# Performance work log

Hardware: AMD Instinct MI355X
Metric: run time of the kernel (lower is better)

Reference implementation:

```python
import jax, jax.numpy as jnp
import numpy as np

N, E = 50000, 800000
IN_C, HID_C, OUT_C, HEADS = 128, 32, 16, 4
NEG_SLOPE = 0.2


def gat_conv(x, src, dst, W, att_src, att_dst, bias, heads, out_ch, concat, n_nodes):
    # linear transform: [N, heads, out_ch]
    h = (x @ W).reshape(n_nodes, heads, out_ch)
    # per-node attention logits [N, heads]
    a_s = (h * att_src).sum(-1)
    a_d = (h * att_dst).sum(-1)
    # per-edge raw attention (edge j->i uses src logit of j, dst logit of i)
    alpha = jax.nn.leaky_relu(a_s[src] + a_d[dst], negative_slope=NEG_SLOPE)  # [E, heads]
    # segment softmax over destination neighborhoods
    amax = jax.ops.segment_max(alpha, dst, num_segments=n_nodes)
    ex = jnp.exp(alpha - amax[dst])
    den = jax.ops.segment_sum(ex, dst, num_segments=n_nodes)
    coef = ex / den[dst]  # [E, heads]
    # weighted scatter-add aggregation
    msg = h[src] * coef[:, :, None]  # [E, heads, out_ch]
    out = jax.ops.segment_sum(msg, dst, num_segments=n_nodes)  # [N, heads, out_ch]
    out = out.reshape(n_nodes, heads * out_ch) if concat else out.mean(axis=1)
    return out + bias


def setup_inputs() -> dict:
    key = jax.random.key(0)
    ks = jax.random.split(key, 10)
    x = jax.random.normal(ks[0], (N, IN_C), dtype=jnp.float32)
    edge_index = jax.random.randint(ks[1], (2, E), 0, N, dtype=jnp.int64)
    s1 = 1.0 / np.sqrt(IN_C)
    s2 = 1.0 / np.sqrt(HID_C * HEADS)
    W1 = jax.random.normal(ks[2], (IN_C, HEADS * HID_C), dtype=jnp.float32) * s1
    att_src1 = jax.random.normal(ks[3], (HEADS, HID_C), dtype=jnp.float32) * s1
    att_dst1 = jax.random.normal(ks[4], (HEADS, HID_C), dtype=jnp.float32) * s1
    b1 = jnp.zeros((HEADS * HID_C,), dtype=jnp.float32)
    W2 = jax.random.normal(ks[5], (HEADS * HID_C, OUT_C), dtype=jnp.float32) * s2
    att_src2 = jax.random.normal(ks[6], (1, OUT_C), dtype=jnp.float32) * s2
    att_dst2 = jax.random.normal(ks[7], (1, OUT_C), dtype=jnp.float32) * s2
    b2 = jnp.zeros((OUT_C,), dtype=jnp.float32)
    return {"x": x, "edge_index": edge_index, "W1": W1, "att_src1": att_src1,
            "att_dst1": att_dst1, "b1": b1, "W2": W2, "att_src2": att_src2,
            "att_dst2": att_dst2, "b2": b2}


def reference(x, edge_index, W1, att_src1, att_dst1, b1, W2, att_src2, att_dst2, b2):
    n = x.shape[0]
    # PyG GATConv default: add self loops
    ar = jnp.arange(n, dtype=edge_index.dtype)
    src = jnp.concatenate([edge_index[0], ar])
    dst = jnp.concatenate([edge_index[1], ar])
    h = gat_conv(x, src, dst, W1, att_src1, att_dst1, b1, HEADS, HID_C, True, n)
    h = jax.nn.elu(h)
    out = gat_conv(h, src, dst, W2, att_src2, att_dst2, b2, 1, OUT_C, False, n)
    return out
```

## Files before the change

### kernel.cpp

```cpp
#include <hip/hip_runtime.h>

typedef __attribute__((ext_vector_type(8))) short short8;
typedef __attribute__((ext_vector_type(4))) float f32x4;
typedef __attribute__((ext_vector_type(2))) float f32x2;

__device__ __forceinline__ float lrelu02(float a) { return a > 0.0f ? a : 0.2f * a; }

__device__ __forceinline__ unsigned bf16rne(float f) {
    unsigned u = __float_as_uint(f);
    return (u + 0x7fffu + ((u >> 16) & 1u)) >> 16;
}

__global__ __launch_bounds__(256) void k_rank(
    const int* __restrict__ ei, int* __restrict__ deg, int* __restrict__ rank,
    int E, int N)
{
    int tid = blockIdx.x * blockDim.x + threadIdx.x;
    int nthr = gridDim.x * blockDim.x;
    int E4 = E & ~3;
    for (int b = tid * 4; b < E4; b += nthr * 4) {
        int4 d = *(const int4*)(ei + E + b);
        int4 r;
        r.x = atomicAdd(&deg[d.x], 1);
        r.y = atomicAdd(&deg[d.y], 1);
        r.z = atomicAdd(&deg[d.z], 1);
        r.w = atomicAdd(&deg[d.w], 1);
        *(int4*)(rank + b) = r;
    }
    for (int e = E4 + tid; e < E; e += nthr)
        rank[e] = atomicAdd(&deg[ei[E + e]], 1);
    for (int i = tid; i < N; i += nthr)
        rank[E + i] = atomicAdd(&deg[i], 1);
}

__global__ __launch_bounds__(256) void k_gemm1(
    const float* __restrict__ x, const float* __restrict__ W,
    const float* __restrict__ attS, const float* __restrict__ attD,
    unsigned short* __restrict__ h1, float* __restrict__ as1, float* __restrict__ ad1,
    int4* __restrict__ degz, int n4, int N)
{
    __shared__ unsigned short Wt[128 * 128];
    __shared__ unsigned short xs[64 * 128];

    const int t = threadIdx.x;
    const int lane = t & 63;
    const int wv = t >> 6;
    const int ln = lane & 15;
    const int lg = lane >> 4;
    const int r0 = blockIdx.x * 64;

    for (int i = blockIdx.x * 256 + t; i < n4; i += gridDim.x * 256)
        degz[i] = make_int4(0, 0, 0, 0);

    #pragma unroll
    for (int i = 0; i < 16; ++i) {
        int flat = i * 256 + t;
        int n = flat & 127;
        int k0 = (flat >> 7) * 4;
        float v0 = W[(size_t)(k0 + 0) * 128 + n];
        float v1 = W[(size_t)(k0 + 1) * 128 + n];
        float v2 = W[(size_t)(k0 + 2) * 128 + n];
        float v3 = W[(size_t)(k0 + 3) * 128 + n];
        uint2 pk;
        pk.x = bf16rne(v0) | (bf16rne(v1) << 16);
        pk.y = bf16rne(v2) | (bf16rne(v3) << 16);
        int byteo = n * 256 + ((k0 * 2) ^ ((n & 7) << 4));
        *(uint2*)((char*)Wt + byteo) = pk;
    }
    {
        int mbase = t >> 5, k0 = (t & 31) * 4;
        #pragma unroll
        for (int it = 0; it < 8; ++it) {
            int m = mbase + it * 8;
            int rr = r0 + m;
            float4 v = make_float4(0.f, 0.f, 0.f, 0.f);
            if (rr < N) v = *(const float4*)&x[(size_t)rr * 128 + k0];
            unsigned lo = bf16rne(v.x) | (bf16rne(v.y) << 16);
            unsigned hi = bf16rne(v.z) | (bf16rne(v.w) << 16);
            int byteo = m * 256 + ((k0 * 2) ^ ((m & 7) << 4));
            *(uint2*)((char*)xs + byteo) = make_uint2(lo, hi);
        }
    }
    __syncthreads();

    f32x4 acc[8];
    #pragma unroll
    for (int i = 0; i < 8; ++i) acc[i] = (f32x4)(0.f);

    #pragma unroll
    for (int kk = 0; kk < 4; ++kk) {
        int kb = (kk * 32 + lg * 8) * 2;
        int am = wv * 16 + ln;
        short8 a = *(const short8*)((char*)xs + am * 256 + (kb ^ ((am & 7) << 4)));
        #pragma unroll
        for (int tile = 0; tile < 8; ++tile) {
            int n = tile * 16 + ln;
            short8 b = *(const short8*)((char*)Wt + n * 256 + (kb ^ ((n & 7) << 4)));
            acc[tile] = __builtin_amdgcn_mfma_f32_16x16x32_bf16(a, b, acc[tile], 0, 0, 0);
        }
    }

    float aSt[8], aDt[8];
    #pragma unroll
    for (int tile = 0; tile < 8; ++tile) {
        aSt[tile] = attS[tile * 16 + ln];
        aDt[tile] = attD[tile * 16 + ln];
    }
    #pragma unroll
    for (int r = 0; r < 4; ++r) {
        int row = r0 + wv * 16 + lg * 4 + r;
        #pragma unroll
        for (int h = 0; h < 4; ++h) {
            float s = acc[2*h][r] * aSt[2*h] + acc[2*h+1][r] * aSt[2*h+1];
            float d = acc[2*h][r] * aDt[2*h] + acc[2*h+1][r] * aDt[2*h+1];
            s += __shfl_xor(s, 1); s += __shfl_xor(s, 2); s += __shfl_xor(s, 4); s += __shfl_xor(s, 8);
            d += __shfl_xor(d, 1); d += __shfl_xor(d, 2); d += __shfl_xor(d, 4); d += __shfl_xor(d, 8);
            if (ln == h * 4 + r && row < N) {
                as1[row * 4 + h] = s;
                ad1[row * 4 + h] = d;
            }
        }
    }

    __syncthreads();
    #pragma unroll
    for (int tile = 0; tile < 8; ++tile) {
        #pragma unroll
        for (int r = 0; r < 4; ++r) {
            int m = wv * 16 + lg * 4 + r;
            int byteo = m * 256 + (((tile * 16 + ln) * 2) ^ ((m & 7) << 4));
            *(unsigned short*)((char*)xs + byteo) = (unsigned short)bf16rne(acc[tile][r]);
        }
    }
    __syncthreads();
    #pragma unroll
    for (int it = 0; it < 4; ++it) {
        int idx = t + it * 256;
        int m = idx >> 4, o = idx & 15;
        int byteo = m * 256 + ((o * 16) ^ ((m & 7) << 4));
        if (r0 + m < N)
            *(uint4*)((char*)(h1 + (size_t)(r0 + m) * 128) + o * 16) =
                *(const uint4*)((const char*)xs + byteo);
    }
}

__global__ __launch_bounds__(256) void k_scan_local(
    const int* __restrict__ deg, int* __restrict__ rowptr, int* __restrict__ bsum, int N)
{
    const int t = threadIdx.x;
    const int base = blockIdx.x * 2048 + t * 8;
    int v[8];
    int s = 0;
    #pragma unroll
    for (int j = 0; j < 8; ++j) {
        int idx = base + j;
        v[j] = (idx < N) ? deg[idx] : 0;
        s += v[j];
    }
    __shared__ int ts[256];
    ts[t] = s;
    __syncthreads();
    #pragma unroll
    for (int off = 1; off < 256; off <<= 1) {
        int u = (t >= off) ? ts[t - off] : 0;
        __syncthreads();
        ts[t] += u;
        __syncthreads();
    }
    int ex = (t == 0) ? 0 : ts[t - 1];
    #pragma unroll
    for (int j = 0; j < 8; ++j) {
        int idx = base + j;
        if (idx < N) rowptr[idx] = ex;
        ex += v[j];
    }
    if (t == 255) bsum[blockIdx.x] = ts[255];
}

__global__ __launch_bounds__(256) void k_scan_add(
    int* __restrict__ rowptr, const int* __restrict__ bsum, int N, int ET)
{
    const int t = threadIdx.x;
    __shared__ int soff;
    if (t < 64) {
        int v = (t < (int)blockIdx.x) ? bsum[t] : 0;
        #pragma unroll
        for (int m = 32; m >= 1; m >>= 1) v += __shfl_xor(v, m);
        if (t == 0) soff = v;
    }
    __syncthreads();
    int off = soff;
    const int base = blockIdx.x * 2048 + t * 8;
    #pragma unroll
    for (int j = 0; j < 8; ++j) {
        int idx = base + j;
        if (idx < N) rowptr[idx] += off;
    }
    if (blockIdx.x == 0 && t == 0) rowptr[N] = ET;
}

__global__ __launch_bounds__(256) void k_fill2(const int* __restrict__ ei,
                                               const int* __restrict__ rank,
                                               const int* __restrict__ rowptr,
                                               int* __restrict__ col, int E, int N) {
    int tid = blockIdx.x * blockDim.x + threadIdx.x;
    int nthr = gridDim.x * blockDim.x;
    int E4 = E & ~3;
    for (int b = tid * 4; b < E4; b += nthr * 4) {
        int4 d = *(const int4*)(ei + E + b);
        int4 s = *(const int4*)(ei + b);
        int4 r = *(const int4*)(rank + b);
        col[rowptr[d.x] + r.x] = s.x;
        col[rowptr[d.y] + r.y] = s.y;
        col[rowptr[d.z] + r.z] = s.z;
        col[rowptr[d.w] + r.w] = s.w;
    }
    for (int e = E4 + tid; e < E; e += nthr)
        col[rowptr[ei[E + e]] + rank[e]] = ei[e];
    for (int i = tid; i < N; i += nthr)
        col[rowptr[i] + rank[E + i]] = i;
}

__global__ __launch_bounds__(256) void k_agg1(
    const unsigned short* __restrict__ h1, const float* __restrict__ as1,
    const float* __restrict__ ad1, const int* __restrict__ rowptr,
    const int* __restrict__ col, const float* __restrict__ b1,
    unsigned short* __restrict__ out1, int N)
{
    int wid = (int)(((unsigned)blockIdx.x * blockDim.x + threadIdx.x) >> 6);
    if (wid >= N) return;
    int lane = threadIdx.x & 63;
    int start = rowptr[wid], end = rowptr[wid + 1];
    int deg = end - start;
    const float4 ad = *(const float4*)(ad1 + (size_t)wid * 4);
    int head = lane >> 4;
    float adh = head == 0 ? ad.x : head == 1 ? ad.y : head == 2 ? ad.z : ad.w;

    f32x2 acc2 = (f32x2)(0.f);

    if (deg <= 64) {
        int idx = lane & 15;
        float ex[4];
        int sv[4];
        float den = 0.f;
        #pragma unroll
        for (int b = 0; b < 4; ++b) {
            int j = b * 16 + idx;
            float v = 0.f;
            int sc = 0;
            if (j < deg) {
                sc = col[start + j];
                v = __expf(lrelu02(as1[(size_t)sc * 4 + head] + adh));
            }
            sv[b] = sc;
            ex[b] = v;
            den += v;
        }
        den += __shfl_xor(den, 1); den += __shfl_xor(den, 2);
        den += __shfl_xor(den, 4); den += __shfl_xor(den, 8);
        float rden = 1.f / den;
        #pragma unroll
        for (int b = 0; b < 4; ++b) ex[b] *= rden;
        int srcbase = lane & 48;

        #pragma unroll
        for (int b = 0; b < 4; ++b) {
            int rem = deg - b * 16;
            if (rem <= 0) break;
            if (rem >= 16) {
                int sq[16]; float cf[16]; unsigned hv[16];
                #pragma unroll
                for (int q = 0; q < 16; ++q) {
                    sq[q] = __builtin_amdgcn_readlane(sv[b], q);
                    cf[q] = __shfl(ex[b], srcbase | q);
                }
                #pragma unroll
                for (int q = 0; q < 16; ++q)
                    hv[q] = *(const unsigned*)(h1 + (size_t)sq[q] * 128 + lane * 2);
                #pragma unroll
                for (int q = 0; q < 16; ++q) {
                    f32x2 h2v;
                    h2v.x = __uint_as_float(hv[q] << 16);
                    h2v.y = __uint_as_float(hv[q] & 0xffff0000u);
                    acc2 += (f32x2)(cf[q]) * h2v;
                }
            } else {
                #pragma unroll
                for (int c4 = 0; c4 < 4; ++c4) {
                    if (c4 * 4 >= rem) break;
                    int sq[4]; float cf[4]; unsigned hv[4];
                    #pragma unroll
                    for (int jj = 0; jj < 4; ++jj) {
                        int q = c4 * 4 + jj;
                        sq[jj] = __builtin_amdgcn_readlane(sv[b], q);
                        cf[jj] = __shfl(ex[b], srcbase | q);
                    }
                    #pragma unroll
                    for (int jj = 0; jj < 4; ++jj)
                        hv[jj] = *(const unsigned*)(h1 + (size_t)sq[jj] * 128 + lane * 2);
                    #pragma unroll
                    for (int jj = 0; jj < 4; ++jj) {
                        f32x2 h2v;
                        h2v.x = __uint_as_float(hv[jj] << 16);
                        h2v.y = __uint_as_float(hv[jj] & 0xffff0000u);
                        acc2 += (f32x2)(cf[jj]) * h2v;
                    }
                }
            }
        }
    } else {
        float den0 = 0.f, den1 = 0.f, den2 = 0.f, den3 = 0.f;
        for (int e = start + lane; e < end; e += 64) {
            int src = col[e];
            const float4 a = *(const float4*)(as1 + (size_t)src * 4);
            den0 += __expf(lrelu02(a.x + ad.x));
            den1 += __expf(lrelu02(a.y + ad.y));
            den2 += __expf(lrelu02(a.z + ad.z));
            den3 += __expf(lrelu02(a.w + ad.w));
        }
        #pragma unroll
        for (int m = 32; m >= 1; m >>= 1) {
            den0 += __shfl_xor(den0, m); den1 += __shfl_xor(den1, m);
            den2 += __shfl_xor(den2, m); den3 += __shfl_xor(den3, m);
        }
        float rden = head == 0 ? 1.f/den0 : head == 1 ? 1.f/den1 : head == 2 ? 1.f/den2 : 1.f/den3;
        for (int e = start; e < end; e += 8) {
            int sq[8]; float av[8], km[8]; unsigned hv[8];
            #pragma unroll
            for (int j = 0; j < 8; ++j) {
                int ee = e + j;
                bool ok = ee < end;
                int es = ok ? ee : e;
                sq[j] = __builtin_amdgcn_readfirstlane(col[es]);
                km[j] = ok ? 1.f : 0.f;
            }
            #pragma unroll
            for (int j = 0; j < 8; ++j)
                av[j] = as1[(size_t)sq[j] * 4 + head];
            #pragma unroll
            for (int j = 0; j < 8; ++j)
                hv[j] = *(const unsigned*)(h1 + (size_t)sq[j] * 128 + lane * 2);
            #pragma unroll
            for (int j = 0; j < 8; ++j) {
                float coef = km[j] * __expf(lrelu02(av[j] + adh)) * rden;
                f32x2 h2v;
                h2v.x = __uint_as_float(hv[j] << 16);
                h2v.y = __uint_as_float(hv[j] & 0xffff0000u);
                acc2 += (f32x2)(coef) * h2v;
            }
        }
    }

    int c0 = lane * 2;
    float o0 = acc2.x + b1[c0];
    float o1 = acc2.y + b1[c0 + 1];
    o0 = o0 > 0.f ? o0 : expm1f(o0);
    o1 = o1 > 0.f ? o1 : expm1f(o1);
    unsigned ov = bf16rne(o0) | (bf16rne(o1) << 16);
    *(unsigned*)((char*)out1 + (size_t)wid * 256 + lane * 4) = ov;
}

__global__ __launch_bounds__(256) void k_gemm2(
    const unsigned short* __restrict__ in, const float* __restrict__ W,
    const float* __restrict__ attS, const float* __restrict__ attD,
    float* __restrict__ h2, float* __restrict__ as2, float* __restrict__ ad2, int N)
{
    __shared__ unsigned short Wt[16 * 128];
    __shared__ unsigned short xs[64 * 128];
    const int t = threadIdx.x;
    const int lane = t & 63;
    const int wv = t >> 6;
    const int ln = lane & 15;
    const int lg = lane >> 4;
    const int r0 = blockIdx.x * 64;

    #pragma unroll
    for (int i = 0; i < 2; ++i) {
        int flat = i * 256 + t;
        int n = flat & 15;
        int k0 = (flat >> 4) * 4;
        float v0 = W[(size_t)(k0 + 0) * 16 + n];
        float v1 = W[(size_t)(k0 + 1) * 16 + n];
        float v2 = W[(size_t)(k0 + 2) * 16 + n];
        float v3 = W[(size_t)(k0 + 3) * 16 + n];
        uint2 pk;
        pk.x = bf16rne(v0) | (bf16rne(v1) << 16);
        pk.y = bf16rne(v2) | (bf16rne(v3) << 16);
        int byteo = n * 256 + ((k0 * 2) ^ ((n & 7) << 4));
        *(uint2*)((char*)Wt + byteo) = pk;
    }
    #pragma unroll
    for (int it = 0; it < 4; ++it) {
        int idx = t + it * 256;
        int m = idx >> 4, o = idx & 15;
        int rr = r0 + m;
        uint4 v = make_uint4(0, 0, 0, 0);
        if (rr < N) v = *(const uint4*)((const char*)(in + (size_t)rr * 128) + o * 16);
        int byteo = m * 256 + ((o * 16) ^ ((m & 7) << 4));
        *(uint4*)((char*)xs + byteo) = v;
    }
    __syncthreads();

    f32x4 acc = (f32x4)(0.f);
    #pragma unroll
    for (int kk = 0; kk < 4; ++kk) {
        int kb = (kk * 32 + lg * 8) * 2;
        int am = wv * 16 + ln;
        short8 a = *(const short8*)((char*)xs + am * 256 + (kb ^ ((am & 7) << 4)));
        short8 b = *(const short8*)((char*)Wt + ln * 256 + (kb ^ ((ln & 7) << 4)));
        acc = __builtin_amdgcn_mfma_f32_16x16x32_bf16(a, b, acc, 0, 0, 0);
    }

    float aSv = attS[ln], aDv = attD[ln];
    #pragma unroll
    for (int r = 0; r < 4; ++r) {
        int row = r0 + wv * 16 + lg * 4 + r;
        float s = acc[r] * aSv;
        float d = acc[r] * aDv;
        s += __shfl_xor(s, 1); s += __shfl_xor(s, 2); s += __shfl_xor(s, 4); s += __shfl_xor(s, 8);
        d += __shfl_xor(d, 1); d += __shfl_xor(d, 2); d += __shfl_xor(d, 4); d += __shfl_xor(d, 8);
        if (row < N) {
            h2[(size_t)row * 16 + ln] = acc[r];
            if (ln == 0) { as2[row] = s; ad2[row] = d; }
        }
    }
}

__global__ __launch_bounds__(256) void k_agg2(
    const float* __restrict__ h2, const float* __restrict__ as2,
    const float* __restrict__ ad2, const int* __restrict__ rowptr,
    const int* __restrict__ col, const float* __restrict__ b2,
    float* __restrict__ out, int N)
{
    int wid = (int)(((unsigned)blockIdx.x * blockDim.x + threadIdx.x) >> 6);
    if (wid >= N) return;
    int lane = threadIdx.x & 63;
    int start = rowptr[wid], end = rowptr[wid + 1];
    int deg = end - start;
    float adv = ad2[wid];
    int sub = lane >> 4, c = lane & 15;
    float acc = 0.f;

    if (deg <= 64) {
        float ex0 = 0.f;
        if (lane < deg) ex0 = __expf(lrelu02(as2[col[start + lane]] + adv));
        float den = ex0;
        #pragma unroll
        for (int m = 32; m >= 1; m >>= 1) den += __shfl_xor(den, m);
        ex0 *= 1.f / den;
        #pragma unroll
        for (int g = 0; g < 4; ++g) {
            if (g * 16 >= deg) break;
            int s[4]; float cf[4], hv[4];
            #pragma unroll
            for (int jj = 0; jj < 4; ++jj) {
                int j = g * 16 + jj * 4 + sub;
                s[jj]  = col[start + (j < deg ? j : 0)];
                cf[jj] = __shfl(ex0, j);
            }
            #pragma unroll
            for (int jj = 0; jj < 4; ++jj)
                hv[jj] = h2[(size_t)s[jj] * 16 + c];
            #pragma unroll
            for (int jj = 0; jj < 4; ++jj)
                acc = fmaf(cf[jj], hv[jj], acc);
        }
    } else {
        float den = 0.f;
        for (int e = start + lane; e < end; e += 64)
            den += __expf(lrelu02(as2[col[e]] + adv));
        #pragma unroll
        for (int m = 32; m >= 1; m >>= 1) den += __shfl_xor(den, m);
        float rden = 1.f / den;
        for (int e0 = start + sub; e0 < end; e0 += 16) {
            int s[4]; float av[4], km[4], hv[4];
            #pragma unroll
            for (int jj = 0; jj < 4; ++jj) {
                int ee = e0 + jj * 4;
                bool ok = ee < end;
                int es = ok ? ee : e0;
                s[jj]  = col[es];
                km[jj] = ok ? 1.f : 0.f;
            }
            #pragma unroll
            for (int jj = 0; jj < 4; ++jj)
                av[jj] = as2[s[jj]];
            #pragma unroll
            for (int jj = 0; jj < 4; ++jj)
                hv[jj] = h2[(size_t)s[jj] * 16 + c];
            #pragma unroll
            for (int jj = 0; jj < 4; ++jj) {
                float coef = km[jj] * __expf(lrelu02(av[jj] + adv)) * rden;
                acc = fmaf(coef, hv[jj], acc);
            }
        }
    }

    acc += __shfl_xor(acc, 16);
    acc += __shfl_xor(acc, 32);
    if (lane < 16) out[(size_t)wid * 16 + lane] = acc + b2[lane];
}

extern "C" void kernel_launch(void* const* d_in, const int* in_sizes, int n_in,
                              void* d_out, int out_size, void* d_ws, size_t ws_size,
                              hipStream_t stream)
{
    const float* x   = (const float*)d_in[0];
    const int*   ei  = (const int*)d_in[1];
    const float* W1  = (const float*)d_in[2];
    const float* aS1 = (const float*)d_in[3];
    const float* aD1 = (const float*)d_in[4];
    const float* b1  = (const float*)d_in[5];
    const float* W2  = (const float*)d_in[6];
    const float* aS2 = (const float*)d_in[7];
    const float* aD2 = (const float*)d_in[8];
    const float* b2  = (const float*)d_in[9];
    float* out = (float*)d_out;

    int N = in_sizes[0] / 128;
    int E = in_sizes[1] / 2;
    int ET = E + N;
    int nblk = (N + 2047) / 2048;
    int G1 = (N + 63) / 64;

    char* w = (char*)d_ws;
    auto alloc = [&](size_t bytes) -> void* {
        void* p = (void*)w;
        w += (bytes + 255) & ~(size_t)255;
        return p;
    };
    unsigned short* h1   = (unsigned short*)alloc((size_t)N * 128 * 2);
    unsigned short* out1 = (unsigned short*)alloc((size_t)N * 128 * 2);
    float* as1   = (float*)alloc((size_t)N * 4 * 4);
    float* ad1   = (float*)alloc((size_t)N * 4 * 4);
    float* h2    = (float*)alloc((size_t)N * 16 * 4);
    float* as2v  = (float*)alloc((size_t)N * 4);
    float* ad2v  = (float*)alloc((size_t)N * 4);
    int* deg     = (int*)alloc((size_t)(N + 4) * 4);
    int* rowptr  = (int*)alloc((size_t)(N + 1) * 4);
    int* rank    = (int*)alloc((size_t)ET * 4);
    int* col     = (int*)alloc((size_t)ET * 4);
    int* bsum    = (int*)alloc(64 * 4);

    const int tb = 256;
    int n4 = (N + 3) / 4;

    k_gemm1 <<<G1, tb, 0, stream>>>(x, W1, aS1, aD1, h1, as1, ad1, (int4*)deg, n4, N);
    k_rank  <<<2048, tb, 0, stream>>>(ei, deg, rank, E, N);
    k_scan_local<<<nblk, tb, 0, stream>>>(deg, rowptr, bsum, N);
    k_scan_add  <<<nblk, tb, 0, stream>>>(rowptr, bsum, N, ET);
    k_fill2     <<<1024, tb, 0, stream>>>(ei, rank, rowptr, col, E, N);

    k_agg1 <<<(N + 3) / 4, tb, 0, stream>>>(h1, as1, ad1, rowptr, col, b1, out1, N);
    k_gemm2<<<G1, tb, 0, stream>>>(out1, W2, aS2, aD2, h2, as2v, ad2v, N);
    k_agg2 <<<(N + 3) / 4, tb, 0, stream>>>(h2, as2v, ad2v, rowptr, col, b2, out, N);
}
```

Measured before the change: 149.4 us.

## Fuse layer-2 linear transform into agg1 and chain the CSR scan

Removes k_gemm2 by computing each node's 16-wide projection h2 = elu(out1) @ W2 inside k_agg1. Each lane multiplies its two channels by W2 rows, and a butterfly of shuffles reduces the result, avoiding the bf16 out1 round trip to memory. Also merges the two scan kernels into one decoupled-lookback scan using a chain array zeroed in gemm1. This saves two launches and the out1 buffer, at the cost of fp32 FMA per wave, extra shuffles and a serial spin between scan blocks.

```diff
diff --git a/kernel.cpp b/kernel.cpp
--- a/kernel.cpp
+++ b/kernel.cpp
@@ -37,7 +37,7 @@
     const float* __restrict__ x, const float* __restrict__ W,
     const float* __restrict__ attS, const float* __restrict__ attD,
     unsigned short* __restrict__ h1, float* __restrict__ as1, float* __restrict__ ad1,
-    int4* __restrict__ degz, int n4, int N)
+    int4* __restrict__ degz, int* __restrict__ chain, int n4, int N)
 {
     __shared__ unsigned short Wt[128 * 128];
     __shared__ unsigned short xs[64 * 128];
@@ -51,6 +51,7 @@
 
     for (int i = blockIdx.x * 256 + t; i < n4; i += gridDim.x * 256)
         degz[i] = make_int4(0, 0, 0, 0);
+    if (blockIdx.x == 0 && t < 64) chain[t] = 0;
 
     #pragma unroll
     for (int i = 0; i < 16; ++i) {
@@ -144,11 +145,13 @@
     }
 }
 
-__global__ __launch_bounds__(256) void k_scan_local(
-    const int* __restrict__ deg, int* __restrict__ rowptr, int* __restrict__ bsum, int N)
+__global__ __launch_bounds__(256) void k_scan(
+    const int* __restrict__ deg, int* __restrict__ rowptr, int* __restrict__ chain,
+    int N, int ET)
 {
     const int t = threadIdx.x;
-    const int base = blockIdx.x * 2048 + t * 8;
+    const int b = blockIdx.x;
+    const int base = b * 2048 + t * 8;
     int v[8];
     int s = 0;
     #pragma unroll
@@ -167,36 +170,28 @@
         ts[t] += u;
         __syncthreads();
     }
-    int ex = (t == 0) ? 0 : ts[t - 1];
+    __shared__ int soff;
+    if (t == 0) {
+        int prev = 0;
+        if (b > 0) {
+            int c;
+            while ((c = __hip_atomic_load(&chain[b - 1], __ATOMIC_ACQUIRE,
+                                          __HIP_MEMORY_SCOPE_AGENT)) == 0) {}
+            prev = c - 1;
+        }
+        __hip_atomic_store(&chain[b], prev + ts[255] + 1, __ATOMIC_RELEASE,
+                           __HIP_MEMORY_SCOPE_AGENT);
+        soff = prev;
+    }
+    __syncthreads();
+    int run = soff + ((t == 0) ? 0 : ts[t - 1]);
     #pragma unroll
     for (int j = 0; j < 8; ++j) {
         int idx = base + j;
-        if (idx < N) rowptr[idx] = ex;
-        ex += v[j];
-    }
-    if (t == 255) bsum[blockIdx.x] = ts[255];
-}
-
-__global__ __launch_bounds__(256) void k_scan_add(
-    int* __restrict__ rowptr, const int* __restrict__ bsum, int N, int ET)
-{
-    const int t = threadIdx.x;
-    __shared__ int soff;
-    if (t < 64) {
-        int v = (t < (int)blockIdx.x) ? bsum[t] : 0;
-        #pragma unroll
-        for (int m = 32; m >= 1; m >>= 1) v += __shfl_xor(v, m);
-        if (t == 0) soff = v;
-    }
-    __syncthreads();
-    int off = soff;
-    const int base = blockIdx.x * 2048 + t * 8;
-    #pragma unroll
-    for (int j = 0; j < 8; ++j) {
-        int idx = base + j;
-        if (idx < N) rowptr[idx] += off;
-    }
-    if (blockIdx.x == 0 && t == 0) rowptr[N] = ET;
+        if (idx < N) rowptr[idx] = run;
+        run += v[j];
+    }
+    if (b == 0 && t == 0) rowptr[N] = ET;
 }
 
 __global__ __launch_bounds__(256) void k_fill2(const int* __restrict__ ei,
@@ -225,7 +220,9 @@
     const unsigned short* __restrict__ h1, const float* __restrict__ as1,
     const float* __restrict__ ad1, const int* __restrict__ rowptr,
     const int* __restrict__ col, const float* __restrict__ b1,
-    unsigned short* __restrict__ out1, int N)
+    const float* __restrict__ W2, const float* __restrict__ attS2,
+    const float* __restrict__ attD2,
+    float* __restrict__ h2, float* __restrict__ as2, float* __restrict__ ad2, int N)
 {
     int wid = (int)(((unsigned)blockIdx.x * blockDim.x + threadIdx.x) >> 6);
     if (wid >= N) return;
@@ -356,74 +353,56 @@
     float o1 = acc2.y + b1[c0 + 1];
     o0 = o0 > 0.f ? o0 : expm1f(o0);
     o1 = o1 > 0.f ? o1 : expm1f(o1);
-    unsigned ov = bf16rne(o0) | (bf16rne(o1) << 16);
-    *(unsigned*)((char*)out1 + (size_t)wid * 256 + lane * 4) = ov;
-}
-
-__global__ __launch_bounds__(256) void k_gemm2(
-    const unsigned short* __restrict__ in, const float* __restrict__ W,
-    const float* __restrict__ attS, const float* __restrict__ attD,
-    float* __restrict__ h2, float* __restrict__ as2, float* __restrict__ ad2, int N)
-{
-    __shared__ unsigned short Wt[16 * 128];
-    __shared__ unsigned short xs[64 * 128];
-    const int t = threadIdx.x;
-    const int lane = t & 63;
-    const int wv = t >> 6;
-    const int ln = lane & 15;
-    const int lg = lane >> 4;
-    const int r0 = blockIdx.x * 64;
-
-    #pragma unroll
-    for (int i = 0; i < 2; ++i) {
-        int flat = i * 256 + t;
-        int n = flat & 15;
-        int k0 = (flat >> 4) * 4;
-        float v0 = W[(size_t)(k0 + 0) * 16 + n];
-        float v1 = W[(size_t)(k0 + 1) * 16 + n];
-        float v2 = W[(size_t)(k0 + 2) * 16 + n];
-        float v3 = W[(size_t)(k0 + 3) * 16 + n];
-        uint2 pk;
-        pk.x = bf16rne(v0) | (bf16rne(v1) << 16);
-        pk.y = bf16rne(v2) | (bf16rne(v3) << 16);
-        int byteo = n * 256 + ((k0 * 2) ^ ((n & 7) << 4));
-        *(uint2*)((char*)Wt + byteo) = pk;
-    }
-    #pragma unroll
-    for (int it = 0; it < 4; ++it) {
-        int idx = t + it * 256;
-        int m = idx >> 4, o = idx & 15;
-        int rr = r0 + m;
-        uint4 v = make_uint4(0, 0, 0, 0);
-        if (rr < N) v = *(const uint4*)((const char*)(in + (size_t)rr * 128) + o * 16);
-        int byteo = m * 256 + ((o * 16) ^ ((m & 7) << 4));
-        *(uint4*)((char*)xs + byteo) = v;
-    }
-    __syncthreads();
-
-    f32x4 acc = (f32x4)(0.f);
-    #pragma unroll
-    for (int kk = 0; kk < 4; ++kk) {
-        int kb = (kk * 32 + lg * 8) * 2;
-        int am = wv * 16 + ln;
-        short8 a = *(const short8*)((char*)xs + am * 256 + (kb ^ ((am & 7) << 4)));
-        short8 b = *(const short8*)((char*)Wt + ln * 256 + (kb ^ ((ln & 7) << 4)));
-        acc = __builtin_amdgcn_mfma_f32_16x16x32_bf16(a, b, acc, 0, 0, 0);
-    }
-
-    float aSv = attS[ln], aDv = attD[ln];
-    #pragma unroll
-    for (int r = 0; r < 4; ++r) {
-        int row = r0 + wv * 16 + lg * 4 + r;
-        float s = acc[r] * aSv;
-        float d = acc[r] * aDv;
-        s += __shfl_xor(s, 1); s += __shfl_xor(s, 2); s += __shfl_xor(s, 4); s += __shfl_xor(s, 8);
-        d += __shfl_xor(d, 1); d += __shfl_xor(d, 2); d += __shfl_xor(d, 4); d += __shfl_xor(d, 8);
-        if (row < N) {
-            h2[(size_t)row * 16 + ln] = acc[r];
-            if (ln == 0) { as2[row] = s; ad2[row] = d; }
-        }
-    }
+
+    const float4* W2v = (const float4*)W2;
+    float p[16];
+    #pragma unroll
+    for (int j = 0; j < 4; ++j) {
+        float4 wa = W2v[(size_t)c0 * 4 + j];
+        float4 wb = W2v[(size_t)(c0 + 1) * 4 + j];
+        p[4*j+0] = o0 * wa.x + o1 * wb.x;
+        p[4*j+1] = o0 * wa.y + o1 * wb.y;
+        p[4*j+2] = o0 * wa.z + o1 * wb.z;
+        p[4*j+3] = o0 * wa.w + o1 * wb.w;
+    }
+    bool hb = lane & 1;
+    float q8[8];
+    #pragma unroll
+    for (int j = 0; j < 8; ++j) {
+        float keep = hb ? p[2*j+1] : p[2*j];
+        float send = hb ? p[2*j]   : p[2*j+1];
+        q8[j] = keep + __shfl_xor(send, 1);
+    }
+    hb = lane & 2;
+    float r4[4];
+    #pragma unroll
+    for (int j = 0; j < 4; ++j) {
+        float keep = hb ? q8[2*j+1] : q8[2*j];
+        float send = hb ? q8[2*j]   : q8[2*j+1];
+        r4[j] = keep + __shfl_xor(send, 2);
+    }
+    hb = lane & 4;
+    float s2[2];
+    #pragma unroll
+    for (int j = 0; j < 2; ++j) {
+        float keep = hb ? r4[2*j+1] : r4[2*j];
+        float send = hb ? r4[2*j]   : r4[2*j+1];
+        s2[j] = keep + __shfl_xor(send, 4);
+    }
+    hb = lane & 8;
+    float tv = (hb ? s2[1] : s2[0]) + __shfl_xor(hb ? s2[0] : s2[1], 8);
+    tv += __shfl_xor(tv, 16);
+    tv += __shfl_xor(tv, 32);
+
+    int cc = lane & 15;
+    if (lane < 16) h2[(size_t)wid * 16 + lane] = tv;
+    float sp = tv * attS2[cc];
+    float dp = tv * attD2[cc];
+    sp += __shfl_xor(sp, 1); sp += __shfl_xor(sp, 2);
+    sp += __shfl_xor(sp, 4); sp += __shfl_xor(sp, 8);
+    dp += __shfl_xor(dp, 1); dp += __shfl_xor(dp, 2);
+    dp += __shfl_xor(dp, 4); dp += __shfl_xor(dp, 8);
+    if (lane == 0) { as2[wid] = sp; ad2[wid] = dp; }
 }
 
 __global__ __launch_bounds__(256) void k_agg2(
@@ -529,8 +508,7 @@
         w += (bytes + 255) & ~(size_t)255;
         return p;
     };
-    unsigned short* h1   = (unsigned short*)alloc((size_t)N * 128 * 2);
-    unsigned short* out1 = (unsigned short*)alloc((size_t)N * 128 * 2);
+    unsigned short* h1 = (unsigned short*)alloc((size_t)N * 128 * 2);
     float* as1   = (float*)alloc((size_t)N * 4 * 4);
     float* ad1   = (float*)alloc((size_t)N * 4 * 4);
     float* h2    = (float*)alloc((size_t)N * 16 * 4);
@@ -540,18 +518,18 @@
     int* rowptr  = (int*)alloc((size_t)(N + 1) * 4);
     int* rank    = (int*)alloc((size_t)ET * 4);
     int* col     = (int*)alloc((size_t)ET * 4);
-    int* bsum    = (int*)alloc(64 * 4);
+    int* chain   = (int*)alloc(64 * 4);
 
     const int tb = 256;
     int n4 = (N + 3) / 4;
 
-    k_gemm1 <<<G1, tb, 0, stream>>>(x, W1, aS1, aD1, h1, as1, ad1, (int4*)deg, n4, N);
-    k_rank  <<<2048, tb, 0, stream>>>(ei, deg, rank, E, N);
-    k_scan_local<<<nblk, tb, 0, stream>>>(deg, rowptr, bsum, N);
-    k_scan_add  <<<nblk, tb, 0, stream>>>(rowptr, bsum, N, ET);
-    k_fill2     <<<1024, tb, 0, stream>>>(ei, rank, rowptr, col, E, N);
-
-    k_agg1 <<<(N + 3) / 4, tb, 0, stream>>>(h1, as1, ad1, rowptr, col, b1, out1, N);
-    k_gemm2<<<G1, tb, 0, stream>>>(out1, W2, aS2, aD2, h2, as2v, ad2v, N);
+    k_gemm1<<<G1, tb, 0, stream>>>(x, W1, aS1, aD1, h1, as1, ad1,
+                                   (int4*)deg, chain, n4, N);
+    k_rank <<<2048, tb, 0, stream>>>(ei, deg, rank, E, N);
+    k_scan <<<nblk, tb, 0, stream>>>(deg, rowptr, chain, N, ET);
+    k_fill2<<<1024, tb, 0, stream>>>(ei, rank, rowptr, col, E, N);
+
+    k_agg1 <<<(N + 3) / 4, tb, 0, stream>>>(h1, as1, ad1, rowptr, col, b1,
+                                            W2, aS2, aD2, h2, as2v, ad2v, N);
     k_agg2 <<<(N + 3) / 4, tb, 0, stream>>>(h2, as2v, ad2v, rowptr, col, b2, out, N);
 }
```

Result: slower. 189.6 us (+26.9%).
